# Optimization experiments

Hardware: AMD Instinct MI355X
Metric: run time of the kernel (lower is better)

Reference implementation:

```python
import jax, jax.numpy as jnp
import numpy as np

EPS = 1e-6      # torch F.pairwise_distance default eps (added to the difference)
MARGIN = 0.5


def setup_inputs() -> dict:
    key = jax.random.key(0)
    k1, k2 = jax.random.split(key)
    batch = jax.random.normal(k1, (8192, 1024), dtype=jnp.float32)
    positive = jax.random.normal(k2, (1024,), dtype=jnp.float32)
    return {"batch": batch, "positive": positive}


def _loss(batch, positive):
    n, d = batch.shape
    # torch pairwise_distance(x, y) = ||x - y + eps||_2, so
    # ||a - b + eps||^2 = ||a||^2 + ||b||^2 - 2 a.b + 2*eps*(sum(a) - sum(b)) + d*eps^2
    sq = jnp.sum(batch * batch, axis=-1)                 # [n]
    dots = batch @ batch.T                               # [n, n] GEMM
    sums = jnp.sum(batch, axis=-1)                       # [n]
    d2 = (sq[:, None] + sq[None, :] - 2.0 * dots
          + 2.0 * EPS * (sums[:, None] - sums[None, :]) + d * EPS * EPS)
    # exclude self (the python loop concatenates batch[:i], batch[i+1:])
    neg_inf = jnp.asarray(-jnp.inf, d2.dtype)
    d2_masked = jnp.where(jnp.eye(n, dtype=bool), neg_inf, d2)
    max_neg = jnp.sqrt(jnp.maximum(jnp.max(d2_masked, axis=-1), 0.0))  # [n]
    # distance anchor -> positive (with torch eps convention)
    diff = batch - positive[None, :] + EPS
    pos_dist = jnp.sqrt(jnp.sum(diff * diff, axis=-1))   # [n]
    losses = jax.nn.relu(pos_dist - max_neg + MARGIN)    # [n]
    # anchors exactly equal to the positive are skipped in the original loop
    valid = ~jnp.all(batch == positive[None, :], axis=-1)
    cnt = jnp.sum(valid.astype(losses.dtype))
    return jnp.sum(jnp.where(valid, losses, 0.0)) / cnt


def reference(batch, positive):
    return _loss(batch, positive)
```

## Files before the change

kernel.cpp:

```cpp
#include <hip/hip_runtime.h>
#include <hip/hip_bf16.h>


#define NROWS 8192
#define DIM   1024
#define BT    256
#define BKQ   32
#define NT    (DIM / BKQ)
#define NBT   (NROWS / BT)
#define NTRI  (NBT * (NBT + 1) / 2)

constexpr float EPS = 1e-6f;
constexpr float MARGIN = 0.5f;

typedef __attribute__((ext_vector_type(8))) short short8;
typedef __attribute__((ext_vector_type(4))) float f32x4;

__device__ __forceinline__ unsigned short f2bf_rne(float f) {
    unsigned u = __float_as_uint(f);
    u += 0x7fffu + ((u >> 16) & 1u);
    return (unsigned short)(u >> 16);
}

__global__ void prep_kernel(const float* __restrict__ X, const float* __restrict__ P,
                            unsigned short* __restrict__ Xb,
                            float* __restrict__ cj, float* __restrict__ basei,
                            float* __restrict__ posd, int* __restrict__ valid)
{
    const int tid  = threadIdx.x;
    const int w    = tid >> 6;
    const int lane = tid & 63;
    const int row  = blockIdx.x * 4 + w;
    const float* xr = X + (size_t)row * DIM;

    float sq = 0.f, sm = 0.f, pd = 0.f;
    bool eq = true;
    #pragma unroll
    for (int it = 0; it < 4; ++it) {
        const int idx = it * 256 + lane * 4;
        const float4 x = *(const float4*)(xr + idx);
        const float4 p = *(const float4*)(P + idx);
        sq += x.x*x.x + x.y*x.y + x.z*x.z + x.w*x.w;
        sm += x.x + x.y + x.z + x.w;
        const float d0 = x.x - p.x + EPS, d1 = x.y - p.y + EPS;
        const float d2 = x.z - p.z + EPS, d3 = x.w - p.w + EPS;
        pd += d0*d0 + d1*d1 + d2*d2 + d3*d3;
        eq = eq && (x.x == p.x) && (x.y == p.y) && (x.z == p.z) && (x.w == p.w);
        ushort4 b;
        b.x = f2bf_rne(x.x); b.y = f2bf_rne(x.y); b.z = f2bf_rne(x.z); b.w = f2bf_rne(x.w);
        *(ushort4*)(Xb + (size_t)row * DIM + idx) = b;
    }
    #pragma unroll
    for (int off = 32; off >= 1; off >>= 1) {
        sq += __shfl_xor(sq, off);
        sm += __shfl_xor(sm, off);
        pd += __shfl_xor(pd, off);
    }
    const bool alleq = __all(eq);
    if (lane == 0) {
        cj[row]    = sq - 2.f * EPS * sm;
        basei[row] = sq + 2.f * EPS * sm + (float)DIM * EPS * EPS;
        posd[row]  = sqrtf(pd);
        valid[row] = alleq ? 0 : 1;
    }
}

__global__ __launch_bounds__(512, 2) void gemm_max_kernel(
        const unsigned short* __restrict__ Xb,
        const float* __restrict__ cj,
        float* __restrict__ partmax)
{
    __shared__ alignas(16) unsigned short lds[4][16384];
    __shared__ float partrow[4][BT];
    __shared__ float partcol[2][BT];

    const int tid  = threadIdx.x;
    const int lane = tid & 63;
    const int wid  = tid >> 6;
    const int wm   = wid >> 2;
    const int wn   = wid & 3;
    const int l15  = lane & 15;
    const int lk   = lane >> 4;
    const int swz  = lk ^ (l15 >> 2);

    const int t0 = (blockIdx.x & 7) * (NTRI / 8) + (blockIdx.x >> 3);
    int bm = (int)(32.5f - sqrtf(1056.25f - 2.f * (float)t0));
    if (bm < 0) bm = 0;
    if (bm > NBT - 1) bm = NBT - 1;
    while (bm > 0 && (65 * bm - bm * bm) / 2 > t0) --bm;
    while ((65 * (bm + 1) - (bm + 1) * (bm + 1)) / 2 <= t0) ++bm;
    const int bn = bm + (t0 - (65 * bm - bm * bm) / 2);
    const bool diag = (bm == bn);
    const int Mbase = bm * BT, Nbase = bn * BT;

    f32x4 acc[8][4];
    #pragma unroll
    for (int m = 0; m < 8; ++m)
        #pragma unroll
        for (int n = 0; n < 4; ++n)
            acc[m][n] = (f32x4){0.f, 0.f, 0.f, 0.f};

    #define STAGE(MAT_BASE, LDSOFF, T, BI) do {                                              \
        const int k0_ = (T) * BKQ;                                                           \
        _Pragma("unroll")                                                                    \
        for (int inst_ = 0; inst_ < 2; ++inst_) {                                            \
            const int q_   = inst_ * 512 + tid;                                              \
            const int row_ = q_ >> 2;                                                        \
            const int cc_  = (q_ & 3) ^ ((q_ >> 4) & 3);                                     \
            const unsigned short* src_ = Xb + (size_t)((MAT_BASE) + row_) * DIM + k0_ + cc_ * 8; \
            unsigned short* dst_ = &lds[BI][(LDSOFF) + (inst_ * 512 + wid * 64) * 8];        \
            __builtin_amdgcn_global_load_lds((const __attribute__((address_space(1))) void*)src_, \
                                             (__attribute__((address_space(3))) void*)dst_, 16, 0, 0); \
        }                                                                                    \
    } while (0)

    STAGE(Mbase, 0, 0, 0); STAGE(Nbase, 8192, 0, 0);
    STAGE(Mbase, 0, 1, 1); STAGE(Nbase, 8192, 1, 1);
    STAGE(Mbase, 0, 2, 2); STAGE(Nbase, 8192, 2, 2);
    asm volatile("s_waitcnt vmcnt(8)" ::: "memory");
    __builtin_amdgcn_s_barrier();
    __builtin_amdgcn_sched_barrier(0);

    for (int t = 0; t < NT; ++t) {
        const int bi = t & 3;
        const unsigned short* Ab = &lds[bi][0];
        const unsigned short* Bb = &lds[bi][8192];
        const bool st = (t + 3 < NT);
        const int bs = (t + 3) & 3;

        short8 bf[4], af[4];
        #pragma unroll
        for (int n = 0; n < 4; ++n) {
            const int row = wn * 64 + n * 16 + l15;
            bf[n] = *(const short8*)(Bb + (row * 4 + swz) * 8);
        }
        #pragma unroll
        for (int m = 0; m < 4; ++m) {
            const int row = wm * 128 + m * 16 + l15;
            af[m] = *(const short8*)(Ab + (row * 4 + swz) * 8);
        }
        if (st) STAGE(Mbase, 0, t + 3, bs);
        __builtin_amdgcn_s_barrier();
        __builtin_amdgcn_s_setprio(1);
        #pragma unroll
        for (int m = 0; m < 4; ++m)
            #pragma unroll
            for (int n = 0; n < 4; ++n)
                acc[m][n] = __builtin_amdgcn_mfma_f32_16x16x32_bf16(af[m], bf[n], acc[m][n], 0, 0, 0);
        __builtin_amdgcn_s_setprio(0);
        __builtin_amdgcn_s_barrier();

        #pragma unroll
        for (int m = 0; m < 4; ++m) {
            const int row = wm * 128 + (m + 4) * 16 + l15;
            af[m] = *(const short8*)(Ab + (row * 4 + swz) * 8);
        }
        if (st) STAGE(Nbase, 8192, t + 3, bs);
        __builtin_amdgcn_s_barrier();
        __builtin_amdgcn_s_setprio(1);
        #pragma unroll
        for (int m = 0; m < 4; ++m)
            #pragma unroll
            for (int n = 0; n < 4; ++n)
                acc[m + 4][n] = __builtin_amdgcn_mfma_f32_16x16x32_bf16(af[m], bf[n], acc[m + 4][n], 0, 0, 0);
        __builtin_amdgcn_s_setprio(0);

        if (t < NT - 3)       asm volatile("s_waitcnt vmcnt(8)" ::: "memory");
        else if (t == NT - 3) asm volatile("s_waitcnt vmcnt(4)" ::: "memory");
        else                  asm volatile("s_waitcnt vmcnt(0)" ::: "memory");
        __builtin_amdgcn_s_barrier();
        __builtin_amdgcn_sched_barrier(0);
    }
    #undef STAGE

    float cv[4];
    #pragma unroll
    for (int n = 0; n < 4; ++n)
        cv[n] = cj[Nbase + wn * 64 + n * 16 + l15];

    #pragma unroll
    for (int m = 0; m < 8; ++m) {
        #pragma unroll
        for (int r = 0; r < 4; ++r) {
            const int lrow = wm * 128 + m * 16 + lk * 4 + r;
            float v = -__builtin_inff();
            #pragma unroll
            for (int n = 0; n < 4; ++n) {
                float val = cv[n] - 2.f * acc[m][n][r];
                if (diag && lrow == wn * 64 + n * 16 + l15) val = -__builtin_inff();
                v = fmaxf(v, val);
            }
            #pragma unroll
            for (int off = 8; off >= 1; off >>= 1)
                v = fmaxf(v, __shfl_xor(v, off));
            if (l15 == 0) partrow[wn][lrow] = v;
        }
    }

    if (!diag) {
        float vt[4];
        #pragma unroll
        for (int n = 0; n < 4; ++n) vt[n] = -__builtin_inff();
        #pragma unroll
        for (int m = 0; m < 8; ++m) {
            #pragma unroll
            for (int r = 0; r < 4; ++r) {
                const float ci = cj[Mbase + wm * 128 + m * 16 + lk * 4 + r];
                #pragma unroll
                for (int n = 0; n < 4; ++n)
                    vt[n] = fmaxf(vt[n], ci - 2.f * acc[m][n][r]);
            }
        }
        #pragma unroll
        for (int n = 0; n < 4; ++n) {
            vt[n] = fmaxf(vt[n], __shfl_xor(vt[n], 16));
            vt[n] = fmaxf(vt[n], __shfl_xor(vt[n], 32));
            if (lk == 0) partcol[wm][wn * 64 + n * 16 + l15] = vt[n];
        }
    }
    __syncthreads();

    if (tid < BT) {
        const float v = fmaxf(fmaxf(partrow[0][tid], partrow[1][tid]),
                              fmaxf(partrow[2][tid], partrow[3][tid]));
        partmax[(size_t)bn * NROWS + Mbase + tid] = v;
    } else if (!diag) {
        const int c = tid - BT;
        partmax[(size_t)bm * NROWS + Nbase + c] = fmaxf(partcol[0][c], partcol[1][c]);
    }
}

__global__ void finalize1_kernel(const float* __restrict__ partmax,
                                 const float* __restrict__ basei,
                                 const float* __restrict__ posd,
                                 const int* __restrict__ valid,
                                 float* __restrict__ partials)
{
    const int tid = threadIdx.x;
    const int row = blockIdx.x * 256 + tid;
    float m = -__builtin_inff();
    #pragma unroll 8
    for (int p = 0; p < NBT; ++p)
        m = fmaxf(m, partmax[(size_t)p * NROWS + row]);
    const float d2 = m + basei[row];
    const float mn = sqrtf(fmaxf(d2, 0.f));
    float loss = fmaxf(posd[row] - mn + MARGIN, 0.f);
    float cnt = 1.f;
    if (!valid[row]) { loss = 0.f; cnt = 0.f; }
    #pragma unroll
    for (int off = 32; off >= 1; off >>= 1) {
        loss += __shfl_xor(loss, off);
        cnt  += __shfl_xor(cnt, off);
    }
    __shared__ float sl[4], sc[4];
    const int w = tid >> 6, lane = tid & 63;
    if (lane == 0) { sl[w] = loss; sc[w] = cnt; }
    __syncthreads();
    if (tid == 0) {
        partials[blockIdx.x * 2]     = sl[0] + sl[1] + sl[2] + sl[3];
        partials[blockIdx.x * 2 + 1] = sc[0] + sc[1] + sc[2] + sc[3];
    }
}

__global__ void finalize2_kernel(const float* __restrict__ partials, float* __restrict__ out)
{
    const int tid = threadIdx.x;
    float l = 0.f, c = 0.f;
    if (tid < 32) { l = partials[tid * 2]; c = partials[tid * 2 + 1]; }
    #pragma unroll
    for (int off = 32; off >= 1; off >>= 1) {
        l += __shfl_xor(l, off);
        c += __shfl_xor(c, off);
    }
    if (tid == 0) out[0] = l / c;
}

extern "C" void kernel_launch(void* const* d_in, const int* in_sizes, int n_in,
                              void* d_out, int out_size, void* d_ws, size_t ws_size,
                              hipStream_t stream)
{
    const float* X = (const float*)d_in[0];
    const float* P = (const float*)d_in[1];
    float* out = (float*)d_out;
    char* ws = (char*)d_ws;

    unsigned short* Xb = (unsigned short*)ws;
    size_t off = (size_t)NROWS * DIM * sizeof(unsigned short);
    float* cj    = (float*)(ws + off);  off += (size_t)NROWS * 4;
    float* basei = (float*)(ws + off);  off += (size_t)NROWS * 4;
    float* posd  = (float*)(ws + off);  off += (size_t)NROWS * 4;
    int*   valid = (int*)(ws + off);    off += (size_t)NROWS * 4;
    float* partmax = (float*)(ws + off); off += (size_t)NBT * NROWS * 4;
    float* partials = (float*)(ws + off);

    prep_kernel<<<NROWS / 4, 256, 0, stream>>>(X, P, Xb, cj, basei, posd, valid);
    gemm_max_kernel<<<NTRI, 512, 0, stream>>>(Xb, cj, partmax);
    finalize1_kernel<<<NROWS / 256, 256, 0, stream>>>(partmax, basei, posd, valid, partials);
    finalize2_kernel<<<1, 64, 0, stream>>>(partials, out);
}
```

Baseline: 137.8 us.

## Restructure GEMM main loop to BK=64 double-buffered quadrant pipeline

Changes the K tile from 32 to 64 and replaces the 4-deep ring of stages with a double buffer split into four 128-row slots. The per-iteration work becomes four MFMA phases over accumulator quadrants, with the next tile's slot loads interleaved between phases. It also switches to an 8-way XOR swizzle suited to 64-element rows. The aim is to halve the number of loop iterations and barriers per unit of K and to improve overlap, at the cost of shallower prefetch depth and more register pressure from larger fragment sets.

```diff
diff --git a/kernel.cpp b/kernel.cpp
--- a/kernel.cpp
+++ b/kernel.cpp
@@ -5,8 +5,8 @@
 #define NROWS 8192
 #define DIM   1024
 #define BT    256
-#define BKQ   32
-#define NT    (DIM / BKQ)
+#define BK    64
+#define NKT   (DIM / BK)
 #define NBT   (NROWS / BT)
 #define NTRI  (NBT * (NBT + 1) / 2)
 
@@ -70,7 +70,7 @@
         const float* __restrict__ cj,
         float* __restrict__ partmax)
 {
-    __shared__ alignas(16) unsigned short lds[4][16384];
+    __shared__ alignas(16) unsigned short lds[2][4][8192];
     __shared__ float partrow[4][BT];
     __shared__ float partcol[2][BT];
 
@@ -81,7 +81,8 @@
     const int wn   = wid & 3;
     const int l15  = lane & 15;
     const int lk   = lane >> 4;
-    const int swz  = lk ^ (l15 >> 2);
+    const int cx0  = lk ^ (l15 & 7);
+    const int cx1  = (4 + lk) ^ (l15 & 7);
 
     const int t0 = (blockIdx.x & 7) * (NTRI / 8) + (blockIdx.x >> 3);
     int bm = (int)(32.5f - sqrtf(1056.25f - 2.f * (float)t0));
@@ -100,74 +101,108 @@
         for (int n = 0; n < 4; ++n)
             acc[m][n] = (f32x4){0.f, 0.f, 0.f, 0.f};
 
-    #define STAGE(MAT_BASE, LDSOFF, T, BI) do {                                              \
-        const int k0_ = (T) * BKQ;                                                           \
-        _Pragma("unroll")                                                                    \
-        for (int inst_ = 0; inst_ < 2; ++inst_) {                                            \
-            const int q_   = inst_ * 512 + tid;                                              \
-            const int row_ = q_ >> 2;                                                        \
-            const int cc_  = (q_ & 3) ^ ((q_ >> 4) & 3);                                     \
-            const unsigned short* src_ = Xb + (size_t)((MAT_BASE) + row_) * DIM + k0_ + cc_ * 8; \
-            unsigned short* dst_ = &lds[BI][(LDSOFF) + (inst_ * 512 + wid * 64) * 8];        \
+    #define STAGE(BUF, SLOT, GBASE, KT) do {                                                  \
+        _Pragma("unroll")                                                                     \
+        for (int inst_ = 0; inst_ < 2; ++inst_) {                                             \
+            const int q_ = inst_ * 512 + tid;                                                 \
+            const int r_ = q_ >> 3;                                                           \
+            const int c_ = (q_ & 7) ^ (r_ & 7);                                               \
+            const unsigned short* src_ = Xb + (size_t)((GBASE) + r_) * DIM + (KT) * BK + c_ * 8; \
+            unsigned short* dst_ = &lds[BUF][SLOT][(inst_ * 512 + wid * 64) * 8];             \
             __builtin_amdgcn_global_load_lds((const __attribute__((address_space(1))) void*)src_, \
                                              (__attribute__((address_space(3))) void*)dst_, 16, 0, 0); \
-        }                                                                                    \
+        }                                                                                     \
     } while (0)
 
-    STAGE(Mbase, 0, 0, 0); STAGE(Nbase, 8192, 0, 0);
-    STAGE(Mbase, 0, 1, 1); STAGE(Nbase, 8192, 1, 1);
-    STAGE(Mbase, 0, 2, 2); STAGE(Nbase, 8192, 2, 2);
+    STAGE(0, 0, Mbase, 0); STAGE(0, 1, Mbase + 128, 0);
+    STAGE(0, 2, Nbase, 0); STAGE(0, 3, Nbase + 128, 0);
+    STAGE(1, 0, Mbase, 1); STAGE(1, 1, Mbase + 128, 1);
+    STAGE(1, 2, Nbase, 1); STAGE(1, 3, Nbase + 128, 1);
     asm volatile("s_waitcnt vmcnt(8)" ::: "memory");
     __builtin_amdgcn_s_barrier();
     __builtin_amdgcn_sched_barrier(0);
 
-    for (int t = 0; t < NT; ++t) {
-        const int bi = t & 3;
-        const unsigned short* Ab = &lds[bi][0];
-        const unsigned short* Bb = &lds[bi][8192];
-        const bool st = (t + 3 < NT);
-        const int bs = (t + 3) & 3;
-
-        short8 bf[4], af[4];
-        #pragma unroll
-        for (int n = 0; n < 4; ++n) {
-            const int row = wn * 64 + n * 16 + l15;
-            bf[n] = *(const short8*)(Bb + (row * 4 + swz) * 8);
-        }
-        #pragma unroll
-        for (int m = 0; m < 4; ++m) {
-            const int row = wm * 128 + m * 16 + l15;
-            af[m] = *(const short8*)(Ab + (row * 4 + swz) * 8);
-        }
-        if (st) STAGE(Mbase, 0, t + 3, bs);
+    const int cl0 = (wn & 1) * 64;
+
+    for (int kt = 0; kt < NKT; ++kt) {
+        const int b = kt & 1;
+        const unsigned short* Ah = &lds[b][wm][0];
+        const unsigned short* Bh = &lds[b][2 + (wn >> 1)][0];
+        const bool st = (kt + 2 < NKT);
+        const int kp = kt + 2;
+        short8 af[8], bf0[4], bf1[4];
+
+        #pragma unroll
+        for (int mt = 0; mt < 4; ++mt) {
+            af[mt * 2]     = *(const short8*)(Ah + (mt * 16 + l15) * 64 + cx0 * 8);
+            af[mt * 2 + 1] = *(const short8*)(Ah + (mt * 16 + l15) * 64 + cx1 * 8);
+        }
+        #pragma unroll
+        for (int nt = 0; nt < 2; ++nt) {
+            bf0[nt * 2]     = *(const short8*)(Bh + (cl0 + nt * 16 + l15) * 64 + cx0 * 8);
+            bf0[nt * 2 + 1] = *(const short8*)(Bh + (cl0 + nt * 16 + l15) * 64 + cx1 * 8);
+        }
         __builtin_amdgcn_s_barrier();
         __builtin_amdgcn_s_setprio(1);
         #pragma unroll
-        for (int m = 0; m < 4; ++m)
-            #pragma unroll
-            for (int n = 0; n < 4; ++n)
-                acc[m][n] = __builtin_amdgcn_mfma_f32_16x16x32_bf16(af[m], bf[n], acc[m][n], 0, 0, 0);
+        for (int mt = 0; mt < 4; ++mt)
+            #pragma unroll
+            for (int nt = 0; nt < 2; ++nt)
+                #pragma unroll
+                for (int ks = 0; ks < 2; ++ks)
+                    acc[mt][nt] = __builtin_amdgcn_mfma_f32_16x16x32_bf16(af[mt*2+ks], bf0[nt*2+ks], acc[mt][nt], 0, 0, 0);
         __builtin_amdgcn_s_setprio(0);
         __builtin_amdgcn_s_barrier();
 
         #pragma unroll
-        for (int m = 0; m < 4; ++m) {
-            const int row = wm * 128 + (m + 4) * 16 + l15;
-            af[m] = *(const short8*)(Ab + (row * 4 + swz) * 8);
-        }
-        if (st) STAGE(Nbase, 8192, t + 3, bs);
+        for (int nt = 0; nt < 2; ++nt) {
+            bf1[nt * 2]     = *(const short8*)(Bh + (cl0 + 32 + nt * 16 + l15) * 64 + cx0 * 8);
+            bf1[nt * 2 + 1] = *(const short8*)(Bh + (cl0 + 32 + nt * 16 + l15) * 64 + cx1 * 8);
+        }
+        if (st) STAGE(b, 2, Nbase, kp);
         __builtin_amdgcn_s_barrier();
         __builtin_amdgcn_s_setprio(1);
         #pragma unroll
-        for (int m = 0; m < 4; ++m)
-            #pragma unroll
-            for (int n = 0; n < 4; ++n)
-                acc[m + 4][n] = __builtin_amdgcn_mfma_f32_16x16x32_bf16(af[m], bf[n], acc[m + 4][n], 0, 0, 0);
+        for (int mt = 0; mt < 4; ++mt)
+            #pragma unroll
+            for (int nt = 0; nt < 2; ++nt)
+                #pragma unroll
+                for (int ks = 0; ks < 2; ++ks)
+                    acc[mt][2+nt] = __builtin_amdgcn_mfma_f32_16x16x32_bf16(af[mt*2+ks], bf1[nt*2+ks], acc[mt][2+nt], 0, 0, 0);
         __builtin_amdgcn_s_setprio(0);
-
-        if (t < NT - 3)       asm volatile("s_waitcnt vmcnt(8)" ::: "memory");
-        else if (t == NT - 3) asm volatile("s_waitcnt vmcnt(4)" ::: "memory");
-        else                  asm volatile("s_waitcnt vmcnt(0)" ::: "memory");
+        __builtin_amdgcn_s_barrier();
+
+        #pragma unroll
+        for (int mt = 0; mt < 4; ++mt) {
+            af[mt * 2]     = *(const short8*)(Ah + (64 + mt * 16 + l15) * 64 + cx0 * 8);
+            af[mt * 2 + 1] = *(const short8*)(Ah + (64 + mt * 16 + l15) * 64 + cx1 * 8);
+        }
+        if (st) STAGE(b, 3, Nbase + 128, kp);
+        __builtin_amdgcn_s_barrier();
+        __builtin_amdgcn_s_setprio(1);
+        #pragma unroll
+        for (int mt = 0; mt < 4; ++mt)
+            #pragma unroll
+            for (int nt = 0; nt < 2; ++nt)
+                #pragma unroll
+                for (int ks = 0; ks < 2; ++ks)
+                    acc[4+mt][2+nt] = __builtin_amdgcn_mfma_f32_16x16x32_bf16(af[mt*2+ks], bf1[nt*2+ks], acc[4+mt][2+nt], 0, 0, 0);
+        __builtin_amdgcn_s_setprio(0);
+        __builtin_amdgcn_s_barrier();
+
+        if (st) { STAGE(b, 0, Mbase, kp); STAGE(b, 1, Mbase + 128, kp); }
+        __builtin_amdgcn_s_setprio(1);
+        #pragma unroll
+        for (int mt = 0; mt < 4; ++mt)
+            #pragma unroll
+            for (int nt = 0; nt < 2; ++nt)
+                #pragma unroll
+                for (int ks = 0; ks < 2; ++ks)
+                    acc[4+mt][nt] = __builtin_amdgcn_mfma_f32_16x16x32_bf16(af[mt*2+ks], bf0[nt*2+ks], acc[4+mt][nt], 0, 0, 0);
+        __builtin_amdgcn_s_setprio(0);
+
+        if (kt < NKT - 2)       asm volatile("s_waitcnt vmcnt(8)" ::: "memory");
+        else if (kt == NKT - 2) asm volatile("s_waitcnt vmcnt(0)" ::: "memory");
         __builtin_amdgcn_s_barrier();
         __builtin_amdgcn_sched_barrier(0);
     }
```

New measurement: 127.8 us. 7.3% less time.
